# Performance work log

Measured on AMD Instinct MI355X. Metric: run time of the kernel, lower is better.

The kernel has to match this reference:

```python
import jax, jax.numpy as jnp
import numpy as np

N_NODES = 20000
N_EDGES = 320000
IN_DIM = 64
H = 8      # num_heads
D = 16     # h_dim (out_dim)
CLAMP = 5.0


def setup_inputs() -> dict:
    key = jax.random.key(0)
    ks = jax.random.split(key, 12)
    inp = {
        'x': jax.random.normal(ks[0], (N_NODES, IN_DIM), jnp.float32),
        'edge_attr': jax.random.normal(ks[1], (N_EDGES, IN_DIM), jnp.float32),
        'edge_index': jax.random.randint(ks[2], (2, N_EDGES), 0, N_NODES),
        'Qw': jax.random.normal(ks[3], (IN_DIM, H * D), jnp.float32) * 0.1,
        'Qb': jnp.zeros((H * D,), jnp.float32),
        'Kw': jax.random.normal(ks[4], (IN_DIM, H * D), jnp.float32) * 0.1,
        'Kb': jnp.zeros((H * D,), jnp.float32),
        'Ew': jax.random.normal(ks[5], (IN_DIM, H * D * 2), jnp.float32) * 0.1,
        'Eb': jnp.zeros((H * D * 2,), jnp.float32),
        'Vw': jax.random.normal(ks[6], (IN_DIM, H * D), jnp.float32) * 0.1,
        'Vb': jnp.zeros((H * D,), jnp.float32),
        'Aw': jax.random.normal(ks[7], (D, H, 1), jnp.float32) * 0.1,
        'VeRow': jax.random.normal(ks[8], (D, H, D), jnp.float32) * 0.1,
    }
    return inp


def reference(x, edge_attr, edge_index, Qw, Qb, Kw, Kb, Ew, Eb, Vw, Vb, Aw, VeRow):
    N = x.shape[0]
    Ne = edge_attr.shape[0]
    src, dst = edge_index[0], edge_index[1]

    # node/edge projections (torch Linear stored as [in, out])
    Q_h = (x @ Qw + Qb).reshape(N, H, D)
    K_h = (x @ Kw + Kb).reshape(N, H, D)
    V_h = (x @ Vw + Vb).reshape(N, H, D)
    E = (edge_attr @ Ew + Eb).reshape(Ne, H, 2 * D)
    Ex1, Ex2 = E[:, :, :D], E[:, :, D:]

    # edge-wise additive score with signed-sqrt edge term  [Ne, H, D]
    s2 = Ex1 * Ex2
    score = K_h[src] + Q_h[dst] + jnp.sqrt(jax.nn.relu(s2)) - jnp.sqrt(jax.nn.relu(-s2))
    e_t = score
    oE = score.reshape(Ne, H * D)

    # attention logits: contract with Aw, clamp  [Ne, H, 1]
    a = jnp.einsum('ehd,dhc->ehc', score, Aw)
    a = jnp.clip(a, -CLAMP, CLAMP)

    # segment softmax over destination nodes
    m = jax.ops.segment_max(a, dst, num_segments=N)
    ea = jnp.exp(a - m[dst])
    denom = jax.ops.segment_sum(ea, dst, num_segments=N)
    attn = ea / (denom[dst] + 1e-16)  # [Ne, H, 1]

    # message passing: scatter-add to destination nodes
    oV = jax.ops.segment_sum(V_h[src] * attn, dst, num_segments=N)      # [N, H, D]
    rowV = jax.ops.segment_sum(e_t * attn, dst, num_segments=N)          # [N, H, D]
    rowV = jnp.einsum('nhd,dhc->nhc', rowV, VeRow)
    n_out = (oV + rowV).reshape(N, H * D)
    return n_out, oE
```

## Files before the change

kernel.cpp:

```cpp
#include <hip/hip_runtime.h>

#define IN_DIM 64
#define H 8
#define D 16
#define HD 128
#define CLAMP_V 5.0f
#define ECHUNK 8

__global__ void __launch_bounds__(128) qkv_kernel(
    const float* __restrict__ x,
    const float* __restrict__ Qw, const float* __restrict__ Qb,
    const float* __restrict__ Kw, const float* __restrict__ Kb,
    const float* __restrict__ Vw, const float* __restrict__ Vb,
    float* __restrict__ Q, float* __restrict__ K, float* __restrict__ V)
{
    const int n = blockIdx.x;
    const int t = threadIdx.x;
    __shared__ float xs[IN_DIM];
    if (t < IN_DIM) xs[t] = x[n * IN_DIM + t];
    __syncthreads();
    float aq = Qb[t], ak = Kb[t], av = Vb[t];
#pragma unroll 8
    for (int k = 0; k < IN_DIM; ++k) {
        const float xv = xs[k];
        aq = fmaf(xv, Qw[k * HD + t], aq);
        ak = fmaf(xv, Kw[k * HD + t], ak);
        av = fmaf(xv, Vw[k * HD + t], av);
    }
    Q[n * HD + t] = aq;
    K[n * HD + t] = ak;
    V[n * HD + t] = av;
}

__global__ void zero_kernel(int* __restrict__ p, int n)
{
    const int i = blockIdx.x * blockDim.x + threadIdx.x;
    if (i < n) p[i] = 0;
}

__global__ void count_kernel(const int* __restrict__ ei, int* __restrict__ count, int Ne)
{
    const int e = blockIdx.x * blockDim.x + threadIdx.x;
    if (e < Ne) atomicAdd(&count[ei[Ne + e]], 1);
}

__global__ void __launch_bounds__(1024) scan_kernel(
    const int* __restrict__ count, int* __restrict__ off, int* __restrict__ cursor, int N)
{
    __shared__ int buf[1024];
    __shared__ int stot;
    const int t = threadIdx.x;
    if (t == 0) stot = 0;
    __syncthreads();
    for (int base = 0; base < N; base += 1024) {
        const int v = (base + t < N) ? count[base + t] : 0;
        buf[t] = v;
        __syncthreads();
        for (int s = 1; s < 1024; s <<= 1) {
            const int add = (t >= s) ? buf[t - s] : 0;
            __syncthreads();
            buf[t] += add;
            __syncthreads();
        }
        const int excl = buf[t] - v;
        if (base + t < N) {
            off[base + t]    = stot + excl;
            cursor[base + t] = stot + excl;
        }
        __syncthreads();
        if (t == 1023) stot += buf[1023];
        __syncthreads();
    }
}

__global__ void scatter_kernel(const int* __restrict__ ei, int* __restrict__ cursor,
                               int* __restrict__ elist, int Ne)
{
    const int e = blockIdx.x * blockDim.x + threadIdx.x;
    if (e < Ne) {
        const int dst = ei[Ne + e];
        const int pos = atomicAdd(&cursor[dst], 1);
        elist[pos] = e;
    }
}

__global__ void __launch_bounds__(128) edge_kernel(
    const float* __restrict__ edge_attr, const int* __restrict__ ei,
    const float* __restrict__ Ew, const float* __restrict__ Eb,
    const float* __restrict__ Aw,
    const float* __restrict__ Q, const float* __restrict__ K,
    float* __restrict__ oE, float* __restrict__ ea_ws, int Ne)
{
    const int t = threadIdx.x;
    const int h = t >> 4, d = t & 15;
    const int c1 = h * (2 * D) + d;
    const int c2 = c1 + D;

    __shared__ float xs[ECHUNK][IN_DIM];
    const long e0 = (long)blockIdx.x * ECHUNK;

    for (int i = t; i < ECHUNK * IN_DIM; i += 128) {
        const long gi = e0 * IN_DIM + i;
        xs[i >> 6][i & 63] = (gi < (long)Ne * IN_DIM) ? edge_attr[gi] : 0.0f;
    }
    __syncthreads();

    const float b1 = Eb[c1], b2 = Eb[c2];
    float acc1[ECHUNK], acc2[ECHUNK];
#pragma unroll
    for (int e = 0; e < ECHUNK; ++e) { acc1[e] = b1; acc2[e] = b2; }

#pragma unroll 4
    for (int k = 0; k < IN_DIM; ++k) {
        const float w1 = Ew[k * (2 * H * D) + c1];
        const float w2 = Ew[k * (2 * H * D) + c2];
#pragma unroll
        for (int e = 0; e < ECHUNK; ++e) {
            const float xv = xs[e][k];
            acc1[e] = fmaf(xv, w1, acc1[e]);
            acc2[e] = fmaf(xv, w2, acc2[e]);
        }
    }

    const float aw = Aw[d * H + h];
#pragma unroll
    for (int e = 0; e < ECHUNK; ++e) {
        const int eid = (int)e0 + e;
        if (eid >= Ne) break;
        const int src = ei[eid];
        const int dst = ei[Ne + eid];
        const float s2 = acc1[e] * acc2[e];
        const float ss = copysignf(sqrtf(fabsf(s2)), s2);
        const float score = K[src * HD + t] + Q[dst * HD + t] + ss;
        oE[(long)eid * HD + t] = score;

        float v = score * aw;
        v += __shfl_xor(v, 1);
        v += __shfl_xor(v, 2);
        v += __shfl_xor(v, 4);
        v += __shfl_xor(v, 8);
        if (d == 0) {
            const float a = fminf(fmaxf(v, -CLAMP_V), CLAMP_V);
            ea_ws[(long)eid * H + h] = __expf(a - CLAMP_V);
        }
    }
}

__global__ void __launch_bounds__(128) node_kernel(
    const int* __restrict__ ei, const int* __restrict__ off, const int* __restrict__ count,
    const int* __restrict__ elist,
    const float* __restrict__ V, const float* __restrict__ oE, const float* __restrict__ ea_ws,
    const float* __restrict__ VeRow,
    float* __restrict__ nout, int Ne)
{
    const int n = blockIdx.x;
    const int t = threadIdx.x;
    const int h = t >> 4;
    const int o = off[n], cnt = count[n];

    float accV = 0.0f, accE = 0.0f, den = 0.0f;
    for (int i = 0; i < cnt; ++i) {
        const int e = elist[o + i];
        const int src = ei[e];
        const float ea = ea_ws[(long)e * H + h];
        den += ea;
        accV = fmaf(ea, V[src * HD + t], accV);
        accE = fmaf(ea, oE[(long)e * HD + t], accE);
    }
    const float inv = 1.0f / (den + 1e-16f);
    accV *= inv;
    accE *= inv;

    __shared__ float sE[HD];
    sE[t] = accE;
    __syncthreads();

    float rowv = 0.0f;
    const int hb = h * D;
#pragma unroll
    for (int dp = 0; dp < D; ++dp)
        rowv = fmaf(sE[hb + dp], VeRow[dp * HD + t], rowv);

    nout[n * HD + t] = accV + rowv;
}

extern "C" void kernel_launch(void* const* d_in, const int* in_sizes, int n_in,
                              void* d_out, int out_size, void* d_ws, size_t ws_size,
                              hipStream_t stream)
{
    const float* x         = (const float*)d_in[0];
    const float* edge_attr = (const float*)d_in[1];
    const int*   ei        = (const int*)d_in[2];
    const float* Qw = (const float*)d_in[3];
    const float* Qb = (const float*)d_in[4];
    const float* Kw = (const float*)d_in[5];
    const float* Kb = (const float*)d_in[6];
    const float* Ew = (const float*)d_in[7];
    const float* Eb = (const float*)d_in[8];
    const float* Vw = (const float*)d_in[9];
    const float* Vb = (const float*)d_in[10];
    const float* Aw = (const float*)d_in[11];
    const float* VeRow = (const float*)d_in[12];

    const int N  = in_sizes[0] / IN_DIM;
    const int Ne = in_sizes[2] / 2;

    char* ws = (char*)d_ws;
    float* Q      = (float*)ws; ws += (size_t)N * HD * 4;
    float* K      = (float*)ws; ws += (size_t)N * HD * 4;
    float* V      = (float*)ws; ws += (size_t)N * HD * 4;
    float* ea     = (float*)ws; ws += (size_t)Ne * H * 4;
    int*   count  = (int*)ws;   ws += (size_t)N * 4;
    int*   off    = (int*)ws;   ws += (size_t)N * 4;
    int*   cursor = (int*)ws;   ws += (size_t)N * 4;
    int*   elist  = (int*)ws;   ws += (size_t)Ne * 4;

    float* nout = (float*)d_out;
    float* oE   = nout + (size_t)N * HD;

    hipLaunchKernelGGL(qkv_kernel, dim3(N), dim3(128), 0, stream,
                       x, Qw, Qb, Kw, Kb, Vw, Vb, Q, K, V);
    hipLaunchKernelGGL(zero_kernel, dim3((N + 255) / 256), dim3(256), 0, stream, count, N);
    hipLaunchKernelGGL(count_kernel, dim3((Ne + 255) / 256), dim3(256), 0, stream, ei, count, Ne);
    hipLaunchKernelGGL(scan_kernel, dim3(1), dim3(1024), 0, stream, count, off, cursor, N);
    hipLaunchKernelGGL(scatter_kernel, dim3((Ne + 255) / 256), dim3(256), 0, stream,
                       ei, cursor, elist, Ne);
    hipLaunchKernelGGL(edge_kernel, dim3((Ne + ECHUNK - 1) / ECHUNK), dim3(128), 0, stream,
                       edge_attr, ei, Ew, Eb, Aw, Q, K, oE, ea, Ne);
    hipLaunchKernelGGL(node_kernel, dim3(N), dim3(128), 0, stream,
                       ei, off, count, elist, V, oE, ea, VeRow, nout, Ne);
}
```

Measured before the change: 682.7 us.

## Use split-bf16 MFMA for edge projection, parallel scan, batched QKV, prefetch

```diff
diff --git a/kernel.cpp b/kernel.cpp
--- a/kernel.cpp
+++ b/kernel.cpp
@@ -5,7 +5,23 @@
 #define D 16
 #define HD 128
 #define CLAMP_V 5.0f
-#define ECHUNK 8
+#define NCHUNK 8
+
+typedef __attribute__((ext_vector_type(8))) short bf16x8;
+typedef __attribute__((ext_vector_type(4))) float f32x4;
+
+__device__ inline unsigned short f2b(float f) {
+    unsigned int u = __float_as_uint(f);
+    u += 0x7FFFu + ((u >> 16) & 1u);
+    return (unsigned short)(u >> 16);
+}
+__device__ inline float b2f(unsigned short h) {
+    return __uint_as_float((unsigned int)h << 16);
+}
+__device__ inline void split2(float f, unsigned short& hi, unsigned short& lo) {
+    hi = f2b(f);
+    lo = f2b(f - b2f(hi));
+}
 
 __global__ void __launch_bounds__(128) qkv_kernel(
     const float* __restrict__ x,
@@ -14,22 +30,48 @@
     const float* __restrict__ Vw, const float* __restrict__ Vb,
     float* __restrict__ Q, float* __restrict__ K, float* __restrict__ V)
 {
-    const int n = blockIdx.x;
-    const int t = threadIdx.x;
-    __shared__ float xs[IN_DIM];
-    if (t < IN_DIM) xs[t] = x[n * IN_DIM + t];
+    const int n0 = blockIdx.x * NCHUNK;
+    const int t = threadIdx.x;
+    __shared__ float xs[NCHUNK][IN_DIM];
+    for (int i = t; i < NCHUNK * IN_DIM; i += 128)
+        xs[i >> 6][i & 63] = x[(size_t)n0 * IN_DIM + i];
     __syncthreads();
-    float aq = Qb[t], ak = Kb[t], av = Vb[t];
-#pragma unroll 8
+
+    const float qb = Qb[t], kb = Kb[t], vb = Vb[t];
+    float aq[NCHUNK], ak[NCHUNK], av[NCHUNK];
+#pragma unroll
+    for (int c = 0; c < NCHUNK; ++c) { aq[c] = qb; ak[c] = kb; av[c] = vb; }
+
+#pragma unroll 4
     for (int k = 0; k < IN_DIM; ++k) {
-        const float xv = xs[k];
-        aq = fmaf(xv, Qw[k * HD + t], aq);
-        ak = fmaf(xv, Kw[k * HD + t], ak);
-        av = fmaf(xv, Vw[k * HD + t], av);
-    }
-    Q[n * HD + t] = aq;
-    K[n * HD + t] = ak;
-    V[n * HD + t] = av;
+        const float wq = Qw[k * HD + t];
+        const float wk = Kw[k * HD + t];
+        const float wv = Vw[k * HD + t];
+#pragma unroll
+        for (int c = 0; c < NCHUNK; ++c) {
+            const float xv = xs[c][k];
+            aq[c] = fmaf(xv, wq, aq[c]);
+            ak[c] = fmaf(xv, wk, ak[c]);
+            av[c] = fmaf(xv, wv, av[c]);
+        }
+    }
+#pragma unroll
+    for (int c = 0; c < NCHUNK; ++c) {
+        Q[(size_t)(n0 + c) * HD + t] = aq[c];
+        K[(size_t)(n0 + c) * HD + t] = ak[c];
+        V[(size_t)(n0 + c) * HD + t] = av[c];
+    }
+}
+
+__global__ void prep_ewt_kernel(const float* __restrict__ Ew, unsigned short* __restrict__ EwT)
+{
+    const int idx = blockIdx.x * 256 + threadIdx.x;
+    const int k = idx >> 8, c = idx & 255;
+    const float w = Ew[idx];
+    unsigned short hi, lo;
+    split2(w, hi, lo);
+    EwT[c * 64 + k] = hi;
+    EwT[16384 + c * 64 + k] = lo;
 }
 
 __global__ void zero_kernel(int* __restrict__ p, int n)
@@ -44,32 +86,47 @@
     if (e < Ne) atomicAdd(&count[ei[Ne + e]], 1);
 }
 
-__global__ void __launch_bounds__(1024) scan_kernel(
-    const int* __restrict__ count, int* __restrict__ off, int* __restrict__ cursor, int N)
-{
-    __shared__ int buf[1024];
-    __shared__ int stot;
-    const int t = threadIdx.x;
-    if (t == 0) stot = 0;
+__global__ void __launch_bounds__(512) scan_block_kernel(
+    const int* __restrict__ count, int* __restrict__ off_part, int* __restrict__ bsum, int N)
+{
+    __shared__ int buf[512];
+    const int t = threadIdx.x;
+    const int g = blockIdx.x * 512 + t;
+    const int v = (g < N) ? count[g] : 0;
+    buf[t] = v;
     __syncthreads();
-    for (int base = 0; base < N; base += 1024) {
-        const int v = (base + t < N) ? count[base + t] : 0;
-        buf[t] = v;
+    for (int s = 1; s < 512; s <<= 1) {
+        const int add = (t >= s) ? buf[t - s] : 0;
         __syncthreads();
-        for (int s = 1; s < 1024; s <<= 1) {
-            const int add = (t >= s) ? buf[t - s] : 0;
-            __syncthreads();
-            buf[t] += add;
-            __syncthreads();
-        }
-        const int excl = buf[t] - v;
-        if (base + t < N) {
-            off[base + t]    = stot + excl;
-            cursor[base + t] = stot + excl;
-        }
+        buf[t] += add;
         __syncthreads();
-        if (t == 1023) stot += buf[1023];
-        __syncthreads();
+    }
+    if (g < N) off_part[g] = buf[t] - v;
+    if (t == 511) bsum[blockIdx.x] = buf[511];
+}
+
+__global__ void __launch_bounds__(64) scan_tops_kernel(int* __restrict__ bsum, int NB)
+{
+    const int t = threadIdx.x;
+    int v = (t < NB) ? bsum[t] : 0;
+    const int orig = v;
+#pragma unroll
+    for (int s = 1; s < 64; s <<= 1) {
+        const int o = __shfl_up(v, s);
+        if (t >= s) v += o;
+    }
+    if (t < NB) bsum[t] = v - orig;
+}
+
+__global__ void __launch_bounds__(512) scan_add_kernel(
+    const int* __restrict__ off_part, const int* __restrict__ bsum,
+    int* __restrict__ off, int* __restrict__ cursor, int N)
+{
+    const int g = blockIdx.x * 512 + threadIdx.x;
+    if (g < N) {
+        const int o = off_part[g] + bsum[g >> 9];
+        off[g] = o;
+        cursor[g] = o;
     }
 }
 
@@ -84,64 +141,97 @@
     }
 }
 
-__global__ void __launch_bounds__(128) edge_kernel(
+__global__ void __launch_bounds__(256) edge_kernel(
     const float* __restrict__ edge_attr, const int* __restrict__ ei,
-    const float* __restrict__ Ew, const float* __restrict__ Eb,
-    const float* __restrict__ Aw,
+    const unsigned short* __restrict__ EwTg,
+    const float* __restrict__ Eb, const float* __restrict__ Aw,
     const float* __restrict__ Q, const float* __restrict__ K,
     float* __restrict__ oE, float* __restrict__ ea_ws, int Ne)
 {
     const int t = threadIdx.x;
-    const int h = t >> 4, d = t & 15;
-    const int c1 = h * (2 * D) + d;
-    const int c2 = c1 + D;
-
-    __shared__ float xs[ECHUNK][IN_DIM];
-    const long e0 = (long)blockIdx.x * ECHUNK;
-
-    for (int i = t; i < ECHUNK * IN_DIM; i += 128) {
-        const long gi = e0 * IN_DIM + i;
-        xs[i >> 6][i & 63] = (gi < (long)Ne * IN_DIM) ? edge_attr[gi] : 0.0f;
-    }
-    __syncthreads();
-
-    const float b1 = Eb[c1], b2 = Eb[c2];
-    float acc1[ECHUNK], acc2[ECHUNK];
-#pragma unroll
-    for (int e = 0; e < ECHUNK; ++e) { acc1[e] = b1; acc2[e] = b2; }
-
-#pragma unroll 4
-    for (int k = 0; k < IN_DIM; ++k) {
-        const float w1 = Ew[k * (2 * H * D) + c1];
-        const float w2 = Ew[k * (2 * H * D) + c2];
-#pragma unroll
-        for (int e = 0; e < ECHUNK; ++e) {
-            const float xv = xs[e][k];
-            acc1[e] = fmaf(xv, w1, acc1[e]);
-            acc2[e] = fmaf(xv, w2, acc2[e]);
+    const int e0 = blockIdx.x * 64;
+    const int lane = t & 63, wid = t >> 6;
+    const int m = lane & 15, q = lane >> 4;
+    const int d = m;
+
+    int sld[4], dld[4];
+#pragma unroll
+    for (int j = 0; j < 4; ++j) {
+        const int el = wid * 16 + q * 4 + j;
+        sld[j] = ei[e0 + el];
+        dld[j] = ei[Ne + e0 + el];
+    }
+
+    const float* ar = edge_attr + (size_t)(e0 + wid * 16 + m) * 64 + q * 8;
+    float av[16];
+    *(float4*)(av)      = *(const float4*)(ar);
+    *(float4*)(av + 4)  = *(const float4*)(ar + 4);
+    *(float4*)(av + 8)  = *(const float4*)(ar + 32);
+    *(float4*)(av + 12) = *(const float4*)(ar + 36);
+    bf16x8 a0h, a0l, a1h, a1l;
+#pragma unroll
+    for (int i = 0; i < 8; ++i) {
+        unsigned short hi, lo;
+        split2(av[i], hi, lo);     a0h[i] = (short)hi; a0l[i] = (short)lo;
+        split2(av[i + 8], hi, lo); a1h[i] = (short)hi; a1l[i] = (short)lo;
+    }
+
+#pragma unroll 2
+    for (int h = 0; h < 8; ++h) {
+        const int c1 = h * 32 + d;
+        const int c2 = c1 + 16;
+        const unsigned short* b1p = EwTg + c1 * 64 + q * 8;
+        const unsigned short* b2p = EwTg + c2 * 64 + q * 8;
+        const bf16x8 b00h = *(const bf16x8*)(b1p);
+        const bf16x8 b01h = *(const bf16x8*)(b1p + 32);
+        const bf16x8 b00l = *(const bf16x8*)(b1p + 16384);
+        const bf16x8 b01l = *(const bf16x8*)(b1p + 16384 + 32);
+        const bf16x8 b10h = *(const bf16x8*)(b2p);
+        const bf16x8 b11h = *(const bf16x8*)(b2p + 32);
+        const bf16x8 b10l = *(const bf16x8*)(b2p + 16384);
+        const bf16x8 b11l = *(const bf16x8*)(b2p + 16384 + 32);
+
+        f32x4 acc1 = {0.f, 0.f, 0.f, 0.f}, acc2 = {0.f, 0.f, 0.f, 0.f};
+        acc1 = __builtin_amdgcn_mfma_f32_16x16x32_bf16(a0h, b00h, acc1, 0, 0, 0);
+        acc1 = __builtin_amdgcn_mfma_f32_16x16x32_bf16(a1h, b01h, acc1, 0, 0, 0);
+        acc1 = __builtin_amdgcn_mfma_f32_16x16x32_bf16(a0l, b00h, acc1, 0, 0, 0);
+        acc1 = __builtin_amdgcn_mfma_f32_16x16x32_bf16(a1l, b01h, acc1, 0, 0, 0);
+        acc1 = __builtin_amdgcn_mfma_f32_16x16x32_bf16(a0h, b00l, acc1, 0, 0, 0);
+        acc1 = __builtin_amdgcn_mfma_f32_16x16x32_bf16(a1h, b01l, acc1, 0, 0, 0);
+        acc2 = __builtin_amdgcn_mfma_f32_16x16x32_bf16(a0h, b10h, acc2, 0, 0, 0);
+        acc2 = __builtin_amdgcn_mfma_f32_16x16x32_bf16(a1h, b11h, acc2, 0, 0, 0);
+        acc2 = __builtin_amdgcn_mfma_f32_16x16x32_bf16(a0l, b10h, acc2, 0, 0, 0);
+        acc2 = __builtin_amdgcn_mfma_f32_16x16x32_bf16(a1l, b11h, acc2, 0, 0, 0);
+        acc2 = __builtin_amdgcn_mfma_f32_16x16x32_bf16(a0h, b10l, acc2, 0, 0, 0);
+        acc2 = __builtin_amdgcn_mfma_f32_16x16x32_bf16(a1h, b11l, acc2, 0, 0, 0);
+
+        const float eb1 = Eb[c1], eb2 = Eb[c2];
+        const float aw = Aw[d * H + h];
+        float eav[4];
+#pragma unroll
+        for (int j = 0; j < 4; ++j) {
+            const int el = wid * 16 + q * 4 + j;
+            const float x1 = acc1[j] + eb1;
+            const float x2 = acc2[j] + eb2;
+            const float s2 = x1 * x2;
+            const float ss = copysignf(sqrtf(fabsf(s2)), s2);
+            const float sc = K[(size_t)sld[j] * HD + h * D + d]
+                           + Q[(size_t)dld[j] * HD + h * D + d] + ss;
+            oE[(size_t)(e0 + el) * HD + h * D + d] = sc;
+            float v = sc * aw;
+            v += __shfl_xor(v, 1);
+            v += __shfl_xor(v, 2);
+            v += __shfl_xor(v, 4);
+            v += __shfl_xor(v, 8);
+            eav[j] = v;
         }
-    }
-
-    const float aw = Aw[d * H + h];
-#pragma unroll
-    for (int e = 0; e < ECHUNK; ++e) {
-        const int eid = (int)e0 + e;
-        if (eid >= Ne) break;
-        const int src = ei[eid];
-        const int dst = ei[Ne + eid];
-        const float s2 = acc1[e] * acc2[e];
-        const float ss = copysignf(sqrtf(fabsf(s2)), s2);
-        const float score = K[src * HD + t] + Q[dst * HD + t] + ss;
-        oE[(long)eid * HD + t] = score;
-
-        float v = score * aw;
-        v += __shfl_xor(v, 1);
-        v += __shfl_xor(v, 2);
-        v += __shfl_xor(v, 4);
-        v += __shfl_xor(v, 8);
         if (d == 0) {
-            const float a = fminf(fmaxf(v, -CLAMP_V), CLAMP_V);
-            ea_ws[(long)eid * H + h] = __expf(a - CLAMP_V);
+#pragma unroll
+            for (int j = 0; j < 4; ++j) {
+                const int el = wid * 16 + q * 4 + j;
+                const float a = fminf(fmaxf(eav[j], -CLAMP_V), CLAMP_V);
+                ea_ws[(size_t)(e0 + el) * H + h] = __expf(a - CLAMP_V);
+            }
         }
     }
 }
@@ -159,13 +249,15 @@
     const int o = off[n], cnt = count[n];
 
     float accV = 0.0f, accE = 0.0f, den = 0.0f;
+    int e_n = 0, s_n = 0;
+    if (cnt > 0) { e_n = elist[o]; s_n = ei[e_n]; }
     for (int i = 0; i < cnt; ++i) {
-        const int e = elist[o + i];
-        const int src = ei[e];
-        const float ea = ea_ws[(long)e * H + h];
-        den += ea;
-        accV = fmaf(ea, V[src * HD + t], accV);
-        accE = fmaf(ea, oE[(long)e * HD + t], accE);
+        const int e = e_n, s = s_n;
+        if (i + 1 < cnt) { e_n = elist[o + i + 1]; s_n = ei[e_n]; }
+        const float w = ea_ws[(size_t)e * H + h];
+        den += w;
+        accV = fmaf(w, V[(size_t)s * HD + t], accV);
+        accE = fmaf(w, oE[(size_t)e * HD + t], accE);
     }
     const float inv = 1.0f / (den + 1e-16f);
     accV *= inv;
@@ -204,29 +296,36 @@
 
     const int N  = in_sizes[0] / IN_DIM;
     const int Ne = in_sizes[2] / 2;
+    const int NB = (N + 511) / 512;
 
     char* ws = (char*)d_ws;
-    float* Q      = (float*)ws; ws += (size_t)N * HD * 4;
-    float* K      = (float*)ws; ws += (size_t)N * HD * 4;
-    float* V      = (float*)ws; ws += (size_t)N * HD * 4;
-    float* ea     = (float*)ws; ws += (size_t)Ne * H * 4;
-    int*   count  = (int*)ws;   ws += (size_t)N * 4;
-    int*   off    = (int*)ws;   ws += (size_t)N * 4;
-    int*   cursor = (int*)ws;   ws += (size_t)N * 4;
-    int*   elist  = (int*)ws;   ws += (size_t)Ne * 4;
+    float* Q       = (float*)ws; ws += (size_t)N * HD * 4;
+    float* K       = (float*)ws; ws += (size_t)N * HD * 4;
+    float* V       = (float*)ws; ws += (size_t)N * HD * 4;
+    float* ea      = (float*)ws; ws += (size_t)Ne * H * 4;
+    int*   count   = (int*)ws;   ws += (size_t)N * 4;
+    int*   off     = (int*)ws;   ws += (size_t)N * 4;
+    int*   cursor  = (int*)ws;   ws += (size_t)N * 4;
+    int*   offp    = (int*)ws;   ws += (size_t)N * 4;
+    int*   elist   = (int*)ws;   ws += (size_t)Ne * 4;
+    int*   bsum    = (int*)ws;   ws += 256;
+    unsigned short* EwT = (unsigned short*)ws; ws += 2 * 16384 * 2;
 
     float* nout = (float*)d_out;
     float* oE   = nout + (size_t)N * HD;
 
-    hipLaunchKernelGGL(qkv_kernel, dim3(N), dim3(128), 0, stream,
+    hipLaunchKernelGGL(prep_ewt_kernel, dim3(64), dim3(256), 0, stream, Ew, EwT);
+    hipLaunchKernelGGL(qkv_kernel, dim3(N / NCHUNK), dim3(128), 0, stream,
                        x, Qw, Qb, Kw, Kb, Vw, Vb, Q, K, V);
     hipLaunchKernelGGL(zero_kernel, dim3((N + 255) / 256), dim3(256), 0, stream, count, N);
     hipLaunchKernelGGL(count_kernel, dim3((Ne + 255) / 256), dim3(256), 0, stream, ei, count, Ne);
-    hipLaunchKernelGGL(scan_kernel, dim3(1), dim3(1024), 0, stream, count, off, cursor, N);
+    hipLaunchKernelGGL(scan_block_kernel, dim3(NB), dim3(512), 0, stream, count, offp, bsum, N);
+    hipLaunchKernelGGL(scan_tops_kernel, dim3(1), dim3(64), 0, stream, bsum, NB);
+    hipLaunchKernelGGL(scan_add_kernel, dim3(NB), dim3(512), 0, stream, offp, bsum, off, cursor, N);
     hipLaunchKernelGGL(scatter_kernel, dim3((Ne + 255) / 256), dim3(256), 0, stream,
                        ei, cursor, elist, Ne);
-    hipLaunchKernelGGL(edge_kernel, dim3((Ne + ECHUNK - 1) / ECHUNK), dim3(128), 0, stream,
-                       edge_attr, ei, Ew, Eb, Aw, Q, K, oE, ea, Ne);
+    hipLaunchKernelGGL(edge_kernel, dim3(Ne / 64), dim3(256), 0, stream,
+                       edge_attr, ei, EwT, Eb, Aw, Q, K, oE, ea, Ne);
     hipLaunchKernelGGL(node_kernel, dim3(N), dim3(128), 0, stream,
                        ei, off, count, elist, V, oE, ea, VeRow, nout, Ne);
 }
```

Result: faster. 582.0 us (-14.7%).
